# Kernel tuning notes

Measured on AMD Instinct MI355X. Metric: run time of the kernel, lower is better.

Reference implementation:

```python
import jax, jax.numpy as jnp
import numpy as np

B, S, CI, E, H, L, V, C = 128, 512, 2, 256, 256, 2, 104, 345


def _gru_dir(x, W_ih, W_hh, b_ih, b_hh):
    # x: [B, S, in]; W_ih: [3H, in]; W_hh: [3H, H]
    h_dim = W_hh.shape[1]
    xp = jnp.einsum('bsi,gi->bsg', x, W_ih) + b_ih  # [B, S, 3H] input gates precomputed

    def step(h, xt):
        gh = h @ W_hh.T + b_hh  # [B, 3H]
        xr, xz, xn = jnp.split(xt, 3, axis=-1)
        hr, hz, hn = jnp.split(gh, 3, axis=-1)
        r = jax.nn.sigmoid(xr + hr)
        z = jax.nn.sigmoid(xz + hz)
        n = jnp.tanh(xn + r * hn)
        h_new = (1.0 - z) * n + z * h
        return h_new, h_new

    h0 = jnp.zeros((x.shape[0], h_dim), x.dtype)
    _, ys = jax.lax.scan(step, h0, jnp.swapaxes(xp, 0, 1))
    return jnp.swapaxes(ys, 0, 1)  # [B, S, H]


def _bigru_layer(x, W_ih, W_hh, b_ih, b_hh):
    # stacked-direction params: leading axis 2 = (fwd, bwd)
    fwd = _gru_dir(x, W_ih[0], W_hh[0], b_ih[0], b_hh[0])
    bwd = _gru_dir(x[:, ::-1], W_ih[1], W_hh[1], b_ih[1], b_hh[1])[:, ::-1]
    return jnp.concatenate([fwd, bwd], axis=-1)  # [B, S, 2H]


def setup_inputs() -> dict:
    key = jax.random.key(0)
    ks = jax.random.split(key, 16)
    k = 1.0 / np.sqrt(H)
    u = lambda kk, shp: jax.random.uniform(kk, shp, jnp.float32, -k, k)
    inp = {
        'coordinate': jax.random.normal(ks[0], (B, S, CI), jnp.float32),
        'flag_bits': jax.random.randint(ks[1], (B, S), 0, V),
        'position_encoding': jax.random.randint(ks[2], (B, S), 0, V),
        'coord_W': u(ks[3], (E, CI)),
        'feat_emb': jax.random.normal(ks[4], (V, E), jnp.float32),
        'W_ih_l0': u(ks[5], (2, 3 * H, E)),
        'W_hh_l0': u(ks[6], (2, 3 * H, H)),
        'b_ih_l0': u(ks[7], (2, 3 * H)),
        'b_hh_l0': u(ks[8], (2, 3 * H)),
        'W_ih_l1': u(ks[9], (2, 3 * H, 2 * H)),
        'W_hh_l1': u(ks[10], (2, 3 * H, H)),
        'b_ih_l1': u(ks[11], (2, 3 * H)),
        'b_hh_l1': u(ks[12], (2, 3 * H)),
        'out_W': u(ks[13], (C, 2 * H)),
        'out_b': u(ks[14], (C,)),
    }
    return inp


def reference(coordinate, flag_bits, position_encoding, coord_W, feat_emb,
              W_ih_l0, W_hh_l0, b_ih_l0, b_hh_l0,
              W_ih_l1, W_hh_l1, b_ih_l1, b_hh_l1, out_W, out_b):
    # embed + sum
    x = jnp.einsum('bsc,ec->bse', coordinate, coord_W) \
        + feat_emb[flag_bits] + feat_emb[position_encoding]
    # 2-layer bidirectional GRU (dropout=0)
    h1 = _bigru_layer(x, W_ih_l0, W_hh_l0, b_ih_l0, b_hh_l0)
    h2 = _bigru_layer(h1, W_ih_l1, W_hh_l1, b_ih_l1, b_hh_l1)
    featur = jnp.concatenate([h2[:, -1, :H], h2[:, -1, H:]], axis=1)  # [B, 2H]
    logits = featur @ out_W.T + out_b  # [B, C]
    return (logits, featur)
```

## Files before the change

### kernel.cpp

```cpp
#include <hip/hip_runtime.h>
#include <stdint.h>

#define B_ 128
#define S_ 512
#define E_ 256
#define H_ 256
#define G3 768
#define C_ 345
#define TC_ 64
#define NCH (S_ / TC_)
#define SLAB 24576

typedef __attribute__((ext_vector_type(8))) short short8;
typedef __attribute__((ext_vector_type(4))) float f32x4;
typedef __attribute__((ext_vector_type(4))) unsigned int uint4_;

__device__ __forceinline__ unsigned short f2bf(float f) {
  union { float f; uint32_t u; } v; v.f = f;
  uint32_t r = v.u + 0x7FFF + ((v.u >> 16) & 1);
  return (unsigned short)(r >> 16);
}
__device__ __forceinline__ float bf2f(unsigned short u) {
  union { uint32_t u; float f; } v; v.u = ((uint32_t)u) << 16; return v.f;
}
__device__ __forceinline__ float sigmf(float x) { return 1.f / (1.f + __expf(-x)); }
__device__ __forceinline__ float tanhf_(float x) { return 2.f / (1.f + __expf(-2.f * x)) - 1.f; }

__device__ __forceinline__ void gload_lds16(const void* g, void* l) {
  __builtin_amdgcn_global_load_lds(
      (const __attribute__((address_space(1))) unsigned int*)g,
      (__attribute__((address_space(3))) unsigned int*)l, 16, 0, 0);
}

__global__ void k_sentinel(float* dout) { dout[0] = 1.0e6f; }

__global__ __launch_bounds__(256) void k_cvt(const float* __restrict__ s,
                                             unsigned short* __restrict__ d, int n) {
  int i = blockIdx.x * blockDim.x + threadIdx.x;
  if (i < n) d[i] = f2bf(s[i]);
}

__global__ __launch_bounds__(256) void k_embed_chunk(
    const float* __restrict__ coord, const int* __restrict__ flag,
    const int* __restrict__ pos, const float* __restrict__ cW,
    const float* __restrict__ femb, unsigned short* __restrict__ xeF,
    unsigned short* __restrict__ xeB, int s0) {
  int gid = blockIdx.x * 256 + threadIdx.x;
  int row = gid >> 5, e0 = (gid & 31) * 8;
  int isB = row >= (TC_ * B_);
  int r = isB ? row - TC_ * B_ : row;
  int lt = r >> 7, b = r & 127;
  int t = isB ? (S_ - 1 - (s0 + lt)) : (s0 + lt);
  size_t src = (size_t)b * S_ + t;
  float c0 = coord[src * 2], c1 = coord[src * 2 + 1];
  int f = flag[src], p = pos[src];
  unsigned short* out = (isB ? xeB : xeF) + (size_t)r * E_;
#pragma unroll
  for (int i = 0; i < 8; i++) {
    int e = e0 + i;
    float v = c0 * cW[e * 2] + c1 * cW[e * 2 + 1] + femb[f * E_ + e] + femb[p * E_ + e];
    out[e] = f2bf(v);
  }
}

__global__ __launch_bounds__(256) void k_gemm_bt(
    const unsigned short* __restrict__ A, const unsigned short* __restrict__ Bm,
    unsigned short* __restrict__ C, const float* __restrict__ bias,
    int M, int N, int K) {
  __shared__ unsigned short As[128 * 32];
  __shared__ unsigned short Bs[128 * 32];
  int nt_ = N >> 7;
  int bx = blockIdx.x % nt_, by = blockIdx.x / nt_;
  int tid = threadIdx.x, lane = tid & 63, w = tid >> 6;
  int wr = (w >> 1) * 64, wc = (w & 1) * 64;
  f32x4 acc[4][4] = {};
  int lr = lane >> 2;
  int lc = (lane & 3) * 8;
  for (int kt = 0; kt < K; kt += 32) {
#pragma unroll
    for (int q = 0; q < 2; q++) {
      int r = w * 32 + q * 16;
      gload_lds16(A + (size_t)(by * 128 + r + lr) * K + kt + lc, &As[r * 32]);
      gload_lds16(Bm + (size_t)(bx * 128 + r + lr) * K + kt + lc, &Bs[r * 32]);
    }
    __syncthreads();
    short8 af[4], bf[4];
#pragma unroll
    for (int i = 0; i < 4; i++)
      af[i] = *(const short8*)&As[(wr + i * 16 + (lane & 15)) * 32 + (lane >> 4) * 8];
#pragma unroll
    for (int i = 0; i < 4; i++)
      bf[i] = *(const short8*)&Bs[(wc + i * 16 + (lane & 15)) * 32 + (lane >> 4) * 8];
#pragma unroll
    for (int i = 0; i < 4; i++)
#pragma unroll
      for (int j = 0; j < 4; j++)
        acc[i][j] = __builtin_amdgcn_mfma_f32_16x16x32_bf16(af[i], bf[j], acc[i][j], 0, 0, 0);
    __syncthreads();
  }
#pragma unroll
  for (int i = 0; i < 4; i++)
#pragma unroll
    for (int j = 0; j < 4; j++)
#pragma unroll
      for (int e = 0; e < 4; e++) {
        int rrow = by * 128 + wr + i * 16 + (lane >> 4) * 4 + e;
        int ccol = bx * 128 + wc + j * 16 + (lane & 15);
        float v = acc[i][j][e] + (bias ? bias[ccol] : 0.f);
        int lt = rrow >> 7, b = rrow & 127;
        int bb = b >> 4;
        int g = ccol >> 8, jj = ccol & 255;
        int jtg = jj >> 4;
        int ln = ((b >> 2) & 3) * 16 + (jj & 15);
        int pe = b & 3;
        char* slab = (char*)C + ((size_t)lt * 8 + bb) * SLAB;
        unsigned short hv = f2bf(v);
        int idx = jtg * 256 + pe * 64 + ln;
        if (g < 2)
          *(unsigned short*)(slab + (idx << 2) + g * 2) = hv;
        else
          *(unsigned short*)(slab + 16384 + (idx << 1)) = hv;
      }
}

__global__ __launch_bounds__(512)
__attribute__((amdgpu_waves_per_eu(2, 2)))
void k_scan_chunk(
    const unsigned short* __restrict__ xpF, const unsigned short* __restrict__ xpB,
    const unsigned short* __restrict__ Whh,
    const float* __restrict__ bhh,
    float* __restrict__ hstate,
    unsigned short* __restrict__ hout,
    int s0, int write_hout) {
  __shared__ __align__(16) char smem[131072];
  char* wlds = smem;
  char* hbf = smem + 65536;
  char* xlds = smem + 65536 + 16384;

  int tid = threadIdx.x, lane = tid & 63, w = tid >> 6;
  int dir = blockIdx.x >> 3;
  int b0 = (blockIdx.x & 7) * 16;

  const unsigned short* Wd = Whh + (size_t)dir * G3 * H_;
  const char* xq = (const char*)(dir ? xpB : xpF) + (size_t)(b0 >> 4) * SLAB;
  const float* bhhd = bhh + dir * G3;
  float* hst = hstate + (size_t)dir * B_ * H_;

  float hreg[2][4];

  if (s0 == 0) {
    for (int i = tid; i < 2048; i += 512) ((uint32_t*)hbf)[i] = 0;
#pragma unroll
    for (int jt = 0; jt < 2; jt++)
#pragma unroll
      for (int e = 0; e < 4; e++) hreg[jt][e] = 0.f;
  } else {
#pragma unroll
    for (int jt = 0; jt < 2; jt++)
#pragma unroll
      for (int e = 0; e < 4; e++) {
        int j = 32 * w + jt * 16 + (lane & 15);
        int br = (lane >> 4) * 4 + e;
        float hv = hst[(size_t)(b0 + br) * H_ + j];
        hreg[jt][e] = hv;
        *(unsigned short*)(hbf + br * 512 + ((j * 2) ^ ((br & 7) << 4))) = f2bf(hv);
      }
  }

  {
#pragma unroll
    for (int q = 0; q < 3; q++) {
      int o = (w * 3 + q) * 1024;
      gload_lds16(xq + o + lane * 16, xlds + o);
    }
  }

  short8 wreg[5][8];
#pragma unroll
  for (int t = 0; t < 5; t++) {
    int g = (t < 4) ? (t >> 1) : 2;
    int jt = (t < 4) ? (t & 1) : 0;
    int grow = g * H_ + 32 * w + jt * 16 + (lane & 15);
#pragma unroll
    for (int kt = 0; kt < 8; kt++)
      wreg[t][kt] = *(const short8*)&Wd[(size_t)grow * H_ + kt * 32 + (lane >> 4) * 8];
  }
#pragma unroll
  for (int t = 0; t < 4; t++)
#pragma unroll
    for (int kt = 0; kt < 8; kt++)
      asm volatile("" : "+a"(wreg[t][kt]));
#pragma unroll
  for (int kt = 0; kt < 8; kt++)
    asm volatile("" : "+v"(wreg[4][kt]));

  {
    int base_row = 2 * H_ + 32 * w + 16;
    char* wt = wlds + w * 8192;
    for (int it = 0; it < 8; it++) {
      int r = it * 2 + (lane >> 5);
      int cb = (lane & 31) * 16;
      uint4_ v = *(const uint4_*)&Wd[(size_t)(base_row + r) * H_ + cb / 2];
      *(uint4_*)(wt + r * 512 + (cb ^ ((r & 7) << 4))) = v;
    }
  }
  float brhh[2][3];
#pragma unroll
  for (int jt = 0; jt < 2; jt++)
#pragma unroll
    for (int g = 0; g < 3; g++)
      brhh[jt][g] = bhhd[g * H_ + 32 * w + jt * 16 + (lane & 15)];
  __syncthreads();

  int p = 0;
  for (int sl = 0; sl < TC_; sl++) {
    {
      int sp = (sl + 1 < TC_) ? sl + 1 : sl;
      const char* gsrc = xq + (size_t)sp * 8 * SLAB;
      char* ldst = xlds + (p ^ 1) * SLAB;
#pragma unroll
      for (int q = 0; q < 3; q++) {
        int o = (w * 3 + q) * 1024;
        gload_lds16(gsrc + o + lane * 16, ldst + o);
      }
    }
    f32x4 acc[6] = {};
    char* hb = hbf + p * 8192;
#pragma unroll
    for (int kt = 0; kt < 8; kt++) {
      int ar = lane & 15;
      int co = (kt * 64 + (lane >> 4) * 16) ^ ((ar & 7) << 4);
      short8 af = *(const short8*)(hb + ar * 512 + co);
      acc[0] = __builtin_amdgcn_mfma_f32_16x16x32_bf16(af, wreg[0][kt], acc[0], 0, 0, 0);
      acc[1] = __builtin_amdgcn_mfma_f32_16x16x32_bf16(af, wreg[1][kt], acc[1], 0, 0, 0);
      acc[2] = __builtin_amdgcn_mfma_f32_16x16x32_bf16(af, wreg[2][kt], acc[2], 0, 0, 0);
      acc[3] = __builtin_amdgcn_mfma_f32_16x16x32_bf16(af, wreg[3][kt], acc[3], 0, 0, 0);
      acc[4] = __builtin_amdgcn_mfma_f32_16x16x32_bf16(af, wreg[4][kt], acc[4], 0, 0, 0);
      short8 bf1 = *(const short8*)(wlds + w * 8192 + ar * 512 + co);
      acc[5] = __builtin_amdgcn_mfma_f32_16x16x32_bf16(af, bf1, acc[5], 0, 0, 0);
    }
    int t = dir ? (S_ - 1 - (s0 + sl)) : (s0 + sl);
    char* hbn = hbf + (p ^ 1) * 8192;
    const char* xl = xlds + p * SLAB;
#pragma unroll
    for (int jt = 0; jt < 2; jt++) {
      int jtg = 2 * w + jt;
      int j = 32 * w + jt * 16 + (lane & 15);
#pragma unroll
      for (int e = 0; e < 4; e++) {
        int br = (lane >> 4) * 4 + e;
        int idx = jtg * 256 + e * 64 + lane;
        uint32_t g01 = *(const uint32_t*)(xl + (idx << 2));
        float xr = bf2f((unsigned short)(g01 & 0xFFFF));
        float xz = bf2f((unsigned short)(g01 >> 16));
        float xn = bf2f(*(const unsigned short*)(xl + 16384 + (idx << 1)));
        float gr = acc[0 + jt][e] + brhh[jt][0];
        float gz = acc[2 + jt][e] + brhh[jt][1];
        float gn = acc[4 + jt][e] + brhh[jt][2];
        float r = sigmf(xr + gr);
        float z = sigmf(xz + gz);
        float n = tanhf_(xn + r * gn);
        float hv = (1.f - z) * n + z * hreg[jt][e];
        hreg[jt][e] = hv;
        *(unsigned short*)(hbn + br * 512 + ((j * 2) ^ ((br & 7) << 4))) = f2bf(hv);
      }
    }
    __syncthreads();
    if (write_hout) {
      const char* hs = hbf + (p ^ 1) * 8192;
      int br = tid >> 5, cj = tid & 31;
      uint4_ v = *(const uint4_*)(hs + br * 512 + ((cj * 16) ^ ((br & 7) << 4)));
      *(uint4_*)(hout + ((size_t)t * B_ + b0 + br) * 512 + dir * H_ + cj * 8) = v;
    }
    p ^= 1;
  }
#pragma unroll
  for (int jt = 0; jt < 2; jt++)
#pragma unroll
    for (int e = 0; e < 4; e++) {
      int j = 32 * w + jt * 16 + (lane & 15);
      int br = (lane >> 4) * 4 + e;
      hst[(size_t)(b0 + br) * H_ + j] = hreg[jt][e];
    }
}

__global__ __launch_bounds__(256) void k_final(
    const unsigned short* __restrict__ h1, const float* __restrict__ hlastf,
    const float* __restrict__ Wih1, const float* __restrict__ bih1,
    const float* __restrict__ bhh1, const float* __restrict__ outW,
    const float* __restrict__ outb, float* __restrict__ dout) {
  typedef __attribute__((ext_vector_type(4))) float f4;
  int b = blockIdx.x, tid = threadIdx.x;
  __shared__ float xt[512];
  __shared__ float feat[512];
  for (int i = tid; i < 512; i += 256)
    xt[i] = bf2f(h1[((size_t)(S_ - 1) * B_ + b) * 512 + i]);
  __syncthreads();
  {
    const float* w0 = Wih1 + (size_t)G3 * 512;
    f4 dr = {0.f, 0.f, 0.f, 0.f}, dz = dr, dn = dr;
    const f4* xv = (const f4*)xt;
    const f4* wr_ = (const f4*)(w0 + (size_t)tid * 512);
    const f4* wz_ = (const f4*)(w0 + (size_t)(H_ + tid) * 512);
    const f4* wn_ = (const f4*)(w0 + (size_t)(2 * H_ + tid) * 512);
    for (int k = 0; k < 128; k++) {
      f4 x = xv[k];
      dr += x * wr_[k]; dz += x * wz_[k]; dn += x * wn_[k];
    }
    float sr = dr[0] + dr[1] + dr[2] + dr[3] + bih1[G3 + tid] + bhh1[G3 + tid];
    float sz = dz[0] + dz[1] + dz[2] + dz[3] + bih1[G3 + H_ + tid] + bhh1[G3 + H_ + tid];
    float sn = dn[0] + dn[1] + dn[2] + dn[3] + bih1[G3 + 2 * H_ + tid];
    float r = sigmf(sr);
    float z = sigmf(sz);
    float n = tanhf_(sn + r * bhh1[G3 + 2 * H_ + tid]);
    feat[H_ + tid] = (1.f - z) * n;
    feat[tid] = hlastf[(size_t)b * H_ + tid];
  }
  __syncthreads();
  for (int c = tid; c < C_; c += 256) {
    const f4* wv = (const f4*)(outW + (size_t)c * 512);
    const f4* fv = (const f4*)feat;
    f4 a = {0.f, 0.f, 0.f, 0.f};
    for (int k = 0; k < 128; k++) a += fv[k] * wv[k];
    dout[(size_t)b * C_ + c] = a[0] + a[1] + a[2] + a[3] + outb[c];
  }
  float* fout = dout + (size_t)B_ * C_;
  for (int i = tid; i < 512; i += 256) fout[(size_t)b * 512 + i] = feat[i];
}

extern "C" void kernel_launch(void* const* d_in, const int* in_sizes, int n_in,
                              void* d_out, int out_size, void* d_ws, size_t ws_size,
                              hipStream_t stream) {
  const float* coord = (const float*)d_in[0];
  const int* flag = (const int*)d_in[1];
  const int* pos = (const int*)d_in[2];
  const float* cW = (const float*)d_in[3];
  const float* femb = (const float*)d_in[4];
  const float* Wih0 = (const float*)d_in[5];
  const float* Whh0 = (const float*)d_in[6];
  const float* bih0 = (const float*)d_in[7];
  const float* bhh0 = (const float*)d_in[8];
  const float* Wih1 = (const float*)d_in[9];
  const float* Whh1 = (const float*)d_in[10];
  const float* bih1 = (const float*)d_in[11];
  const float* bhh1 = (const float*)d_in[12];
  const float* outW = (const float*)d_in[13];
  const float* outb = (const float*)d_in[14];
  float* dout = (float*)d_out;

  char* ws = (char*)d_ws;
  size_t off = 0;
  unsigned short* W0b   = (unsigned short*)(ws + off); off += (size_t)2 * G3 * E_ * 2;
  unsigned short* Whh0b = (unsigned short*)(ws + off); off += (size_t)2 * G3 * H_ * 2;
  unsigned short* W1b   = (unsigned short*)(ws + off); off += (size_t)G3 * 512 * 2;
  unsigned short* Whh1b = (unsigned short*)(ws + off); off += (size_t)G3 * H_ * 2;
  float* hstate0        = (float*)(ws + off);          off += (size_t)2 * B_ * H_ * 4;
  float* hstate1        = (float*)(ws + off);          off += (size_t)B_ * H_ * 4;
  unsigned short* xeF   = (unsigned short*)(ws + off); off += (size_t)TC_ * B_ * E_ * 2;
  unsigned short* xeB   = (unsigned short*)(ws + off); off += (size_t)TC_ * B_ * E_ * 2;
  unsigned short* xpF   = (unsigned short*)(ws + off); off += (size_t)TC_ * 8 * SLAB;
  unsigned short* xpB   = (unsigned short*)(ws + off); off += (size_t)TC_ * 8 * SLAB;
  unsigned short* h1    = (unsigned short*)(ws + off); off += (size_t)S_ * B_ * 512 * 2;

  if (ws_size < off) {
    k_sentinel<<<1, 1, 0, stream>>>(dout);
    return;
  }

  k_cvt<<<(2 * G3 * E_ + 255) / 256, 256, 0, stream>>>(Wih0, W0b, 2 * G3 * E_);
  k_cvt<<<(2 * G3 * H_ + 255) / 256, 256, 0, stream>>>(Whh0, Whh0b, 2 * G3 * H_);
  k_cvt<<<(G3 * 512 + 255) / 256, 256, 0, stream>>>(Wih1, W1b, G3 * 512);
  k_cvt<<<(G3 * H_ + 255) / 256, 256, 0, stream>>>(Whh1, Whh1b, G3 * H_);

  const int MCH = TC_ * B_;
  for (int c = 0; c < NCH; c++) {
    int s0 = c * TC_;
    k_embed_chunk<<<(2 * MCH * 32) / 256, 256, 0, stream>>>(coord, flag, pos, cW, femb,
                                                            xeF, xeB, s0);
    k_gemm_bt<<<(G3 / 128) * (MCH / 128), 256, 0, stream>>>(xeF, W0b, xpF, bih0,
                                                            MCH, G3, E_);
    k_gemm_bt<<<(G3 / 128) * (MCH / 128), 256, 0, stream>>>(xeB, W0b + (size_t)G3 * E_,
                                                            xpB, bih0 + G3, MCH, G3, E_);
    k_scan_chunk<<<16, 512, 0, stream>>>(xpF, xpB, Whh0b, bhh0, hstate0, h1, s0, 1);
  }
  for (int c = 0; c < NCH; c++) {
    int s0 = c * TC_;
    k_gemm_bt<<<(G3 / 128) * (MCH / 128), 256, 0, stream>>>(
        h1 + (size_t)s0 * B_ * 512, W1b, xpF, bih1, MCH, G3, 512);
    k_scan_chunk<<<8, 512, 0, stream>>>(xpF, xpF, Whh1b, bhh1, hstate1, nullptr, s0, 0);
  }
  k_final<<<B_, 256, 0, stream>>>(h1, hstate1, Wih1, bih1, bhh1, outW, outb, dout);
}
```

Measured before the change: 4.550 ms.

## Prefetch input-gate projections directly into registers instead of LDS staging

The GEMM epilogue now writes the precomputed input-gate slab in a lane-contiguous layout, so each lane's four batch-row values sit together. The scan kernel then prefetches the next timestep's gate inputs straight into registers with vector global loads, instead of staging them through a double-buffered LDS region. This removes 48KB of LDS and the LDS reads from the serial recurrence's critical path. In exchange it adds register pressure in a kernel already holding weights in VGPRs and AGPRs, and global load latency is hidden only by one step of compute.

Result: slower. 5.058 ms (+11.2%).

```diff
diff --git a/kernel.cpp b/kernel.cpp
--- a/kernel.cpp
+++ b/kernel.cpp
@@ -14,6 +14,7 @@
 typedef __attribute__((ext_vector_type(8))) short short8;
 typedef __attribute__((ext_vector_type(4))) float f32x4;
 typedef __attribute__((ext_vector_type(4))) unsigned int uint4_;
+typedef __attribute__((ext_vector_type(4))) unsigned short ushort4_;
 
 __device__ __forceinline__ unsigned short f2bf(float f) {
   union { float f; uint32_t u; } v; v.f = f;
@@ -109,17 +110,17 @@
         float v = acc[i][j][e] + (bias ? bias[ccol] : 0.f);
         int lt = rrow >> 7, b = rrow & 127;
         int bb = b >> 4;
+        int pe = b & 3;
+        int bq = (b >> 2) & 3;
         int g = ccol >> 8, jj = ccol & 255;
         int jtg = jj >> 4;
-        int ln = ((b >> 2) & 3) * 16 + (jj & 15);
-        int pe = b & 3;
+        int ln = bq * 16 + (jj & 15);
         char* slab = (char*)C + ((size_t)lt * 8 + bb) * SLAB;
         unsigned short hv = f2bf(v);
-        int idx = jtg * 256 + pe * 64 + ln;
         if (g < 2)
-          *(unsigned short*)(slab + (idx << 2) + g * 2) = hv;
+          *(unsigned short*)(slab + jtg * 1024 + ln * 16 + pe * 4 + g * 2) = hv;
         else
-          *(unsigned short*)(slab + 16384 + (idx << 1)) = hv;
+          *(unsigned short*)(slab + 16384 + jtg * 512 + ln * 8 + pe * 2) = hv;
       }
 }
 
@@ -132,10 +133,9 @@
     float* __restrict__ hstate,
     unsigned short* __restrict__ hout,
     int s0, int write_hout) {
-  __shared__ __align__(16) char smem[131072];
+  __shared__ __align__(16) char smem[81920];
   char* wlds = smem;
   char* hbf = smem + 65536;
-  char* xlds = smem + 65536 + 16384;
 
   int tid = threadIdx.x, lane = tid & 63, w = tid >> 6;
   int dir = blockIdx.x >> 3;
@@ -165,14 +165,6 @@
         hreg[jt][e] = hv;
         *(unsigned short*)(hbf + br * 512 + ((j * 2) ^ ((br & 7) << 4))) = f2bf(hv);
       }
-  }
-
-  {
-#pragma unroll
-    for (int q = 0; q < 3; q++) {
-      int o = (w * 3 + q) * 1024;
-      gload_lds16(xq + o + lane * 16, xlds + o);
-    }
   }
 
   short8 wreg[5][8];
@@ -210,20 +202,28 @@
 #pragma unroll
     for (int g = 0; g < 3; g++)
       brhh[jt][g] = bhhd[g * H_ + 32 * w + jt * 16 + (lane & 15)];
+
+  const char* paddrA0 = xq + (2 * w + 0) * 1024 + lane * 16;
+  const char* paddrA1 = xq + (2 * w + 1) * 1024 + lane * 16;
+  const char* paddrB0 = xq + 16384 + (2 * w + 0) * 512 + lane * 8;
+  const char* paddrB1 = xq + 16384 + (2 * w + 1) * 512 + lane * 8;
+
+  uint4_ cpa0 = *(const uint4_*)paddrA0;
+  uint4_ cpa1 = *(const uint4_*)paddrA1;
+  ushort4_ cpb0 = *(const ushort4_*)paddrB0;
+  ushort4_ cpb1 = *(const ushort4_*)paddrB1;
+
   __syncthreads();
 
   int p = 0;
   for (int sl = 0; sl < TC_; sl++) {
-    {
-      int sp = (sl + 1 < TC_) ? sl + 1 : sl;
-      const char* gsrc = xq + (size_t)sp * 8 * SLAB;
-      char* ldst = xlds + (p ^ 1) * SLAB;
-#pragma unroll
-      for (int q = 0; q < 3; q++) {
-        int o = (w * 3 + q) * 1024;
-        gload_lds16(gsrc + o + lane * 16, ldst + o);
-      }
-    }
+    int sp = (sl + 1 < TC_) ? sl + 1 : sl;
+    size_t soff = (size_t)sp * (8 * SLAB);
+    uint4_ npa0 = *(const uint4_*)(paddrA0 + soff);
+    uint4_ npa1 = *(const uint4_*)(paddrA1 + soff);
+    ushort4_ npb0 = *(const ushort4_*)(paddrB0 + soff);
+    ushort4_ npb1 = *(const ushort4_*)(paddrB1 + soff);
+
     f32x4 acc[6] = {};
     char* hb = hbf + p * 8192;
 #pragma unroll
@@ -241,19 +241,18 @@
     }
     int t = dir ? (S_ - 1 - (s0 + sl)) : (s0 + sl);
     char* hbn = hbf + (p ^ 1) * 8192;
-    const char* xl = xlds + p * SLAB;
 #pragma unroll
     for (int jt = 0; jt < 2; jt++) {
-      int jtg = 2 * w + jt;
       int j = 32 * w + jt * 16 + (lane & 15);
+      uint4_ pa = jt ? cpa1 : cpa0;
+      ushort4_ pb = jt ? cpb1 : cpb0;
 #pragma unroll
       for (int e = 0; e < 4; e++) {
         int br = (lane >> 4) * 4 + e;
-        int idx = jtg * 256 + e * 64 + lane;
-        uint32_t g01 = *(const uint32_t*)(xl + (idx << 2));
+        uint32_t g01 = pa[e];
         float xr = bf2f((unsigned short)(g01 & 0xFFFF));
         float xz = bf2f((unsigned short)(g01 >> 16));
-        float xn = bf2f(*(const unsigned short*)(xl + 16384 + (idx << 1)));
+        float xn = bf2f(pb[e]);
         float gr = acc[0 + jt][e] + brhh[jt][0];
         float gz = acc[2 + jt][e] + brhh[jt][1];
         float gn = acc[4 + jt][e] + brhh[jt][2];
@@ -272,6 +271,7 @@
       uint4_ v = *(const uint4_*)(hs + br * 512 + ((cj * 16) ^ ((br & 7) << 4)));
       *(uint4_*)(hout + ((size_t)t * B_ + b0 + br) * 512 + dir * H_ + cj * 8) = v;
     }
+    cpa0 = npa0; cpa1 = npa1; cpb0 = npb0; cpb1 = npb1;
     p ^= 1;
   }
 #pragma unroll
```
